# Kernel optimization log

Hardware: AMD Instinct MI355X
Metric: run time of the kernel (lower is better)

The kernel has to match this reference:

```python
import jax, jax.numpy as jnp
import numpy as np
import math

E = 2048         # n_embd
H = 16           # num query head pairs (num_heads)
HKV = 8          # num_kv_heads
NREP = H // HKV  # 2
HD = E // H // 2 # head_dim = 64
DEPTH = 12
LAMBDA_INIT = 0.8 - 0.6 * math.exp(-0.3 * DEPTH)
EPS = 1e-6


def setup_inputs() -> dict:
    key = jax.random.key(0)
    ks = jax.random.split(key, 10)
    s = lambda fan_in: 1.0 / np.sqrt(fan_in)
    return {
        "x": jax.random.normal(ks[0], (2, 2048, E), jnp.float32),
        "Wq": jax.random.normal(ks[1], (E, E), jnp.float32) * s(E),
        "Wk": jax.random.normal(ks[2], (E, E // NREP), jnp.float32) * s(E),
        "Wv": jax.random.normal(ks[3], (E, E // NREP), jnp.float32) * s(E),
        "Wo": jax.random.normal(ks[4], (E, E), jnp.float32) * s(E),
        "lam_q1": jax.random.normal(ks[5], (HD,), jnp.float32) * 0.1,
        "lam_k1": jax.random.normal(ks[6], (HD,), jnp.float32) * 0.1,
        "lam_q2": jax.random.normal(ks[7], (HD,), jnp.float32) * 0.1,
        "lam_k2": jax.random.normal(ks[8], (HD,), jnp.float32) * 0.1,
        "g": jnp.ones((2 * HD,), jnp.float32),  # RMSNorm weight
    }


def _rotary(x, cos, sin):
    # x: [B, T, nh, HD]; cos/sin: [T, HD//2]
    d = x.shape[-1] // 2
    x1, x2 = x[..., :d], x[..., d:]
    c = cos[None, :, None, :]
    si = sin[None, :, None, :]
    return jnp.concatenate([x1 * c + x2 * si, -x1 * si + x2 * c], axis=-1)


def reference(x, Wq, Wk, Wv, Wo, lam_q1, lam_k1, lam_q2, lam_k2, g):
    B, T, _ = x.shape
    q = (x @ Wq).reshape(B, T, 2 * H, HD)
    k = (x @ Wk).reshape(B, T, 2 * HKV, HD)
    v = (x @ Wv).reshape(B, T, HKV, 2 * HD)

    inv_freq = 1.0 / (10000.0 ** (jnp.arange(0, HD, 2, dtype=jnp.float32) / HD))
    freqs = jnp.arange(T, dtype=jnp.float32)[:, None] * inv_freq[None, :]
    cos, sin = jnp.cos(freqs), jnp.sin(freqs)
    q = _rotary(q, cos, sin)
    k = _rotary(k, cos, sin)

    q = jnp.transpose(q, (0, 2, 1, 3)) * (HD ** -0.5)   # [B, 2H, T, HD]
    k = jnp.repeat(jnp.transpose(k, (0, 2, 1, 3)), NREP, axis=1)  # [B, 2H, T, HD]
    v = jnp.repeat(jnp.transpose(v, (0, 2, 1, 3)), NREP, axis=1)  # [B, H, T, 2HD]

    scores = jnp.einsum('bhtd,bhsd->bhts', q, k)
    scores = jnp.nan_to_num(scores)
    mask = jnp.triu(jnp.full((T, T), -jnp.inf, scores.dtype), 1)
    scores = scores + mask
    p = jax.nn.softmax(scores.astype(jnp.float32), axis=-1).astype(scores.dtype)

    lam1 = jnp.exp(jnp.sum(lam_q1 * lam_k1))
    lam2 = jnp.exp(jnp.sum(lam_q2 * lam_k2))
    lam = lam1 - lam2 + LAMBDA_INIT

    p = p.reshape(B, H, 2, T, T)
    diff = p[:, :, 0] - lam * p[:, :, 1]               # [B, H, T, T]
    attn = jnp.einsum('bhts,bhsd->bhtd', diff, v)      # [B, H, T, 2HD]

    # RMSNorm over last dim (2*HD)
    attn = attn * jax.lax.rsqrt(jnp.mean(attn * attn, axis=-1, keepdims=True) + EPS) * g
    attn = attn * (1.0 - LAMBDA_INIT)
    attn = jnp.transpose(attn, (0, 2, 1, 3)).reshape(B, T, E)
    return attn @ Wo
```

## Files before the change

kernel.cpp:

```cpp
#include <hip/hip_runtime.h>

#define T_SEQ 2048

typedef __bf16 bf16x8 __attribute__((ext_vector_type(8)));
typedef float f32x4 __attribute__((ext_vector_type(4)));
typedef unsigned short u16;

__device__ __forceinline__ u16 f2b(float f) {
  unsigned u = __float_as_uint(f);
  unsigned r = 0x7fffu + ((u >> 16) & 1u);
  return (u16)((u + r) >> 16);
}
__device__ __forceinline__ float b2f(u16 v) {
  return __uint_as_float(((unsigned)v) << 16);
}
__device__ __forceinline__ f32x4 mfma16(bf16x8 a, bf16x8 b, f32x4 c) {
  return __builtin_amdgcn_mfma_f32_16x16x32_bf16(a, b, c, 0, 0, 0);
}
__device__ __forceinline__ unsigned pkhi(float lo, float hi) {
  return __builtin_amdgcn_perm(__float_as_uint(hi), __float_as_uint(lo), 0x07060302u);
}
#if defined(__has_builtin)
#if __has_builtin(__builtin_amdgcn_exp2f)
#define HAVE_RAW_EXP2 1
#endif
#endif
__device__ __forceinline__ float exp2r(float x) {
#ifdef HAVE_RAW_EXP2
  return __builtin_amdgcn_exp2f(x);
#else
  float r;
  asm("v_exp_f32 %0, %1" : "=v"(r) : "v"(x));
  return r;
#endif
}
__device__ __forceinline__ void glds16(const void* g, void* s) {
  __builtin_amdgcn_global_load_lds(
      (const __attribute__((address_space(1))) void*)(uintptr_t)g,
      (__attribute__((address_space(3))) void*)(unsigned)(uintptr_t)s, 16, 0, 0);
}

__global__ void lam_kernel(const float* __restrict__ q1, const float* __restrict__ k1,
                           const float* __restrict__ q2, const float* __restrict__ k2,
                           float* __restrict__ outp) {
  int l = threadIdx.x;
  float a = q1[l] * k1[l];
  float c = q2[l] * k2[l];
  #pragma unroll
  for (int off = 32; off > 0; off >>= 1) {
    a += __shfl_down(a, off);
    c += __shfl_down(c, off);
  }
  if (l == 0) outp[0] = expf(a) - expf(c) + 0.7836057665316244f;
}

__global__ __launch_bounds__(256) void convert_kernel(const float* __restrict__ in,
                                                      u16* __restrict__ outp, int n) {
  int i = (blockIdx.x * 256 + threadIdx.x) * 4;
  if (i >= n) return;
  float4 v = *(const float4*)(in + i);
  ushort4 pk;
  pk.x = f2b(v.x); pk.y = f2b(v.y); pk.z = f2b(v.z); pk.w = f2b(v.w);
  *(ushort4*)(outp + i) = pk;
}

__global__ __launch_bounds__(256) void transposeW_kernel(const float* __restrict__ Wq,
                                                         const float* __restrict__ Wk,
                                                         const float* __restrict__ Wv,
                                                         const float* __restrict__ Wo,
                                                         u16* __restrict__ outp) {
  __shared__ float tile[32][33];
  const int ro0 = blockIdx.y * 32;
  const int r0 = blockIdx.x * 32;
  const float* src; int C, cbase;
  if (ro0 < 2048)      { src = Wq; C = 2048; cbase = 0; }
  else if (ro0 < 3072) { src = Wk; C = 1024; cbase = 2048; }
  else if (ro0 < 4096) { src = Wv; C = 1024; cbase = 3072; }
  else                 { src = Wo; C = 2048; cbase = 4096; }
  const int cs0 = ro0 - cbase;
  const int tx = threadIdx.x & 31, ty = threadIdx.x >> 5;
  #pragma unroll
  for (int k2 = 0; k2 < 4; k2++)
    tile[ty * 4 + k2][tx] = src[(size_t)(r0 + ty * 4 + k2) * C + cs0 + tx];
  __syncthreads();
  #pragma unroll
  for (int k2 = 0; k2 < 4; k2++)
    outp[(size_t)(ro0 + ty * 4 + k2) * 2048 + r0 + tx] = f2b(tile[tx][ty * 4 + k2]);
}

#define STAGE_HALF(TILE, ROLE, BUF)                                                     \
  do {                                                                                  \
    const u16* sp_ = ((ROLE) == 0 || (ROLE) == 3 ? Ag : Bg) +                           \
                     (size_t)((ROLE) >= 2 ? 128 : 0) * K + (size_t)(TILE) * 64;         \
    u16* dp_ = ((ROLE) == 0 || (ROLE) == 3 ? &As[BUF][0] : &Bs[BUF][0]) +               \
               (((ROLE) >= 2 ? 128 : 0) + w * 8) * 64;                                  \
    glds16(sp_, dp_);                                                                   \
    glds16(sp_ + (size_t)64 * K, dp_ + 4096);                                           \
  } while (0)

#define PHASE(I, J, BUF, NEWA, NEWB, BN, STILE, SROLE, SBUF, DOVM)                      \
  do {                                                                                  \
    if (NEWA) {                                                                         \
      _Pragma("unroll") for (int u_ = 0; u_ < 4; u_++) {                                \
        const int ar_ = ((I) * 4 + u_) * 32 + wm * 16 + l15;                            \
        _Pragma("unroll") for (int kk_ = 0; kk_ < 2; kk_++)                             \
            am[u_][kk_] = *(const bf16x8*)&As[BUF][ar_ * 64 +                           \
                              (((kk_ * 4 + quad) ^ (ar_ & 7)) << 3)];                   \
      }                                                                                 \
    }                                                                                   \
    if (NEWB) {                                                                         \
      _Pragma("unroll") for (int v_ = 0; v_ < 2; v_++) {                                \
        const int br_ = ((J) * 2 + v_) * 64 + wn * 16 + l15;                            \
        _Pragma("unroll") for (int kk_ = 0; kk_ < 2; kk_++)                             \
            BN[v_][kk_] = *(const bf16x8*)&Bs[BUF][br_ * 64 +                           \
                              (((kk_ * 4 + quad) ^ (br_ & 7)) << 3)];                   \
      }                                                                                 \
    }                                                                                   \
    STAGE_HALF(STILE, SROLE, SBUF);                                                     \
    __builtin_amdgcn_s_barrier();                                                       \
    asm volatile("s_waitcnt lgkmcnt(0)" ::: "memory");                                  \
    __builtin_amdgcn_sched_barrier(0);                                                  \
    __builtin_amdgcn_s_setprio(1);                                                      \
    _Pragma("unroll") for (int u_ = 0; u_ < 4; u_++)                                    \
        _Pragma("unroll") for (int v_ = 0; v_ < 2; v_++) {                              \
      acc[(I) * 4 + u_][(J) * 2 + v_] =                                                 \
          mfma16(am[u_][0], BN[v_][0], acc[(I) * 4 + u_][(J) * 2 + v_]);                \
      acc[(I) * 4 + u_][(J) * 2 + v_] =                                                 \
          mfma16(am[u_][1], BN[v_][1], acc[(I) * 4 + u_][(J) * 2 + v_]);                \
    }                                                                                   \
    __builtin_amdgcn_s_setprio(0);                                                      \
    if (DOVM) asm volatile("s_waitcnt vmcnt(6)" ::: "memory");                          \
    __builtin_amdgcn_s_barrier();                                                       \
  } while (0)

__global__ __launch_bounds__(512, 2) void gemm256_kernel(const u16* __restrict__ A,
                                                         const u16* __restrict__ BT,
                                                         u16* __restrict__ C, int N, int K) {
  __shared__ alignas(16) u16 As[2][256 * 64];
  __shared__ alignas(16) u16 Bs[2][256 * 64];
  const int tid = threadIdx.x, w = tid >> 6, lane = tid & 63;
  const int l15 = lane & 15, quad = lane >> 4;
  const int wm = w >> 2, wn = w & 3;
  const int lr = lane >> 3, slot = lane & 7, csw = slot ^ lr;
  const int m0 = blockIdx.y * 256, n0 = blockIdx.x * 256;
  const int nkt = K >> 6;

  f32x4 acc[8][4];
  #pragma unroll
  for (int r = 0; r < 8; r++)
    #pragma unroll
    for (int s = 0; s < 4; s++) acc[r][s] = (f32x4){0.f, 0.f, 0.f, 0.f};

  const u16* Ag = A + (size_t)(m0 + w * 8 + lr) * K + csw * 8;
  const u16* Bg = BT + (size_t)(n0 + w * 8 + lr) * K + csw * 8;

  bf16x8 am[4][2], bn0[2][2], bn1[2][2];

  STAGE_HALF(0, 0, 0); STAGE_HALF(0, 1, 0); STAGE_HALF(0, 2, 0); STAGE_HALF(0, 3, 0);
  STAGE_HALF(1, 0, 1); STAGE_HALF(1, 1, 1); STAGE_HALF(1, 2, 1);
  asm volatile("s_waitcnt vmcnt(6)" ::: "memory");
  __builtin_amdgcn_s_barrier();

  #pragma unroll 1
  for (int t = 0; t < nkt; t += 2) {
    PHASE(0, 0, 0, 1, 1, bn0, t + 1, 3, 1, 0);
    PHASE(0, 1, 0, 0, 1, bn1, t + 2, 0, 0, 0);
    PHASE(1, 0, 0, 1, 0, bn0, t + 2, 1, 0, 0);
    PHASE(1, 1, 0, 0, 0, bn1, t + 2, 2, 0, 1);
    PHASE(0, 0, 1, 1, 1, bn0, t + 2, 3, 0, 0);
    PHASE(0, 1, 1, 0, 1, bn1, t + 3, 0, 1, 0);
    PHASE(1, 0, 1, 1, 0, bn0, t + 3, 1, 1, 0);
    PHASE(1, 1, 1, 0, 0, bn1, t + 3, 2, 1, 1);
  }

  const int crow = m0 + wm * 16 + quad * 4;
  const int ccol = n0 + wn * 16 + l15;
  #pragma unroll
  for (int r = 0; r < 8; r++)
    #pragma unroll
    for (int s = 0; s < 4; s++)
      #pragma unroll
      for (int rr = 0; rr < 4; rr++)
        C[(size_t)(crow + r * 32 + rr) * N + ccol + s * 64] = f2b(acc[r][s][rr]);
}

#define OSTAGE(TILE, CH, BUF)                                                           \
  do {                                                                                  \
    if ((CH) == 0) {                                                                    \
      glds16(Ag + (size_t)(TILE) * 64, &As[BUF][0] + w * 512);                          \
      glds16(Ag + (size_t)64 * K + (size_t)(TILE) * 64, &As[BUF][4096] + w * 512);      \
      glds16(Bg + (size_t)(TILE) * 64, &Bs[BUF][0] + w * 512);                          \
    } else {                                                                            \
      glds16(Bg + (size_t)64 * K + (size_t)(TILE) * 64, &Bs[BUF][4096] + w * 512);      \
      glds16(Bg + (size_t)128 * K + (size_t)(TILE) * 64, &Bs[BUF][8192] + w * 512);     \
      glds16(Bg + (size_t)192 * K + (size_t)(TILE) * 64, &Bs[BUF][12288] + w * 512);    \
    }                                                                                   \
  } while (0)

#define OPHASE(BUF, J, NEWA, STILE, SCH, SBUF, DOVM)                                    \
  do {                                                                                  \
    if (NEWA) {                                                                         \
      _Pragma("unroll") for (int fr_ = 0; fr_ < 4; fr_++) {                             \
        const int ar_ = wm * 64 + fr_ * 16 + l15;                                       \
        _Pragma("unroll") for (int kk_ = 0; kk_ < 2; kk_++)                             \
            am[fr_][kk_] = *(const bf16x8*)&As[BUF][ar_ * 64 +                          \
                               (((kk_ * 4 + quad) ^ (ar_ & 7)) << 3)];                  \
      }                                                                                 \
    }                                                                                   \
    _Pragma("unroll") for (int v_ = 0; v_ < 2; v_++) {                                  \
      const int br_ = ((J) * 2 + v_) * 64 + wn * 16 + l15;                              \
      _Pragma("unroll") for (int kk_ = 0; kk_ < 2; kk_++)                               \
          bn[v_][kk_] = *(const bf16x8*)&Bs[BUF][br_ * 64 +                             \
                            (((kk_ * 4 + quad) ^ (br_ & 7)) << 3)];                     \
    }                                                                                   \
    OSTAGE(STILE, SCH, SBUF);                                                           \
    __builtin_amdgcn_s_barrier();                                                       \
    asm volatile("s_waitcnt lgkmcnt(0)" ::: "memory");                                  \
    __builtin_amdgcn_sched_barrier(0);                                                  \
    __builtin_amdgcn_s_setprio(1);                                                      \
    _Pragma("unroll") for (int fr_ = 0; fr_ < 4; fr_++)                                 \
        _Pragma("unroll") for (int v_ = 0; v_ < 2; v_++) {                              \
      acc[fr_][(J) * 2 + v_] = mfma16(am[fr_][0], bn[v_][0], acc[fr_][(J) * 2 + v_]);   \
      acc[fr_][(J) * 2 + v_] = mfma16(am[fr_][1], bn[v_][1], acc[fr_][(J) * 2 + v_]);   \
    }                                                                                   \
    __builtin_amdgcn_s_setprio(0);                                                      \
    if (DOVM) asm volatile("s_waitcnt vmcnt(3)" ::: "memory");                          \
    __builtin_amdgcn_s_barrier();                                                       \
  } while (0)

__global__ __launch_bounds__(512, 2) void gemm128x256_kernel(const u16* __restrict__ A,
                                                             const u16* __restrict__ BT,
                                                             float* __restrict__ C,
                                                             int N, int K) {
  __shared__ alignas(16) u16 As[2][128 * 64];
  __shared__ alignas(16) u16 Bs[2][256 * 64];
  const int tid = threadIdx.x, w = tid >> 6, lane = tid & 63;
  const int l15 = lane & 15, quad = lane >> 4;
  const int wm = w >> 2, wn = w & 3;
  const int lr = lane >> 3, slot = lane & 7, csw = slot ^ lr;
  const int m0 = blockIdx.y * 128, n0 = blockIdx.x * 256;
  const int nkt = K >> 6;

  f32x4 acc[4][4];
  #pragma unroll
  for (int r = 0; r < 4; r++)
    #pragma unroll
    for (int s = 0; s < 4; s++) acc[r][s] = (f32x4){0.f, 0.f, 0.f, 0.f};

  const u16* Ag = A + (size_t)(m0 + w * 8 + lr) * K + csw * 8;
  const u16* Bg = BT + (size_t)(n0 + w * 8 + lr) * K + csw * 8;

  bf16x8 am[4][2], bn[2][2];

  OSTAGE(0, 0, 0); OSTAGE(0, 1, 0); OSTAGE(1, 0, 1);
  asm volatile("s_waitcnt vmcnt(3)" ::: "memory");
  __builtin_amdgcn_s_barrier();

  #pragma unroll 1
  for (int t = 0; t < nkt; t += 2) {
    OPHASE(0, 0, 1, t + 1, 1, 1, 0);
    OPHASE(0, 1, 0, t + 2, 0, 0, 1);
    OPHASE(1, 0, 1, t + 2, 1, 0, 0);
    OPHASE(1, 1, 0, t + 3, 0, 1, 1);
  }

  const int crow = m0 + wm * 64 + quad * 4;
  #pragma unroll
  for (int r = 0; r < 4; r++)
    #pragma unroll
    for (int s = 0; s < 4; s++) {
      const int col = n0 + s * 64 + wn * 16 + l15;
      #pragma unroll
      for (int rr = 0; rr < 4; rr++)
        C[(size_t)(crow + r * 16 + rr) * N + col] = acc[r][s][rr];
    }
}

__global__ __launch_bounds__(256) void rotab_kernel(float* __restrict__ ct,
                                                    float* __restrict__ st) {
  int idx = blockIdx.x * 256 + threadIdx.x;
  int i = idx & 31, t = idx >> 5;
  float invf = exp2f(-(float)i * 0.4152410118609203f);
  float ang = (float)t * invf;
  ct[idx] = cosf(ang);
  st[idx] = sinf(ang);
}

__global__ __launch_bounds__(256) void rotary_kernel(const u16* __restrict__ qkv,
                                                     const float* __restrict__ ct,
                                                     const float* __restrict__ st,
                                                     u16* __restrict__ Qb,
                                                     u16* __restrict__ Kb, float qscale) {
  int idx = blockIdx.x * 256 + threadIdx.x;
  int i4 = (idx & 7) * 4;
  int bt = (idx >> 3) & 4095;
  int hh = idx >> 15;
  int t = bt & (T_SEQ - 1), b = bt >> 11;
  bool isq = hh < 32;
  int col = isq ? hh * 64 : 2048 + (hh - 32) * 64;
  size_t inb = (size_t)bt * 4096 + col + i4;
  ushort4 xa = *(const ushort4*)(qkv + inb);
  ushort4 xb = *(const ushort4*)(qkv + inb + 32);
  float4 c4 = *(const float4*)(ct + t * 32 + i4);
  float4 s4 = *(const float4*)(st + t * 32 + i4);
  float scale = isq ? qscale : 1.0f;
  ushort4 o1, o2;
  {
    float x1 = b2f(xa.x), x2 = b2f(xb.x);
    o1.x = f2b((x1 * c4.x + x2 * s4.x) * scale);
    o2.x = f2b((x2 * c4.x - x1 * s4.x) * scale);
  }
  {
    float x1 = b2f(xa.y), x2 = b2f(xb.y);
    o1.y = f2b((x1 * c4.y + x2 * s4.y) * scale);
    o2.y = f2b((x2 * c4.y - x1 * s4.y) * scale);
  }
  {
    float x1 = b2f(xa.z), x2 = b2f(xb.z);
    o1.z = f2b((x1 * c4.z + x2 * s4.z) * scale);
    o2.z = f2b((x2 * c4.z - x1 * s4.z) * scale);
  }
  {
    float x1 = b2f(xa.w), x2 = b2f(xb.w);
    o1.w = f2b((x1 * c4.w + x2 * s4.w) * scale);
    o2.w = f2b((x2 * c4.w - x1 * s4.w) * scale);
  }
  u16* outp = isq ? (Qb + (size_t)(b * 32 + hh) * (T_SEQ * 64))
                  : (Kb + (size_t)(b * 16 + hh - 32) * (T_SEQ * 64));
  size_t ob = (size_t)t * 64 + i4;
  *(ushort4*)(outp + ob) = o1;
  *(ushort4*)(outp + ob + 32) = o2;
}

__global__ __launch_bounds__(256) void vtrans_kernel(const u16* __restrict__ qkv,
                                                     u16* __restrict__ outp) {
  __shared__ unsigned tile[32][33];
  int bh = blockIdx.z;
  int t0 = blockIdx.x * 32, dv0 = blockIdx.y * 32;
  int tx = threadIdx.x & 31, ty = threadIdx.x >> 5;
  int bt_base = (bh >> 3) * T_SEQ;
  int col = 3072 + (bh & 7) * 128 + dv0 + tx;
  #pragma unroll
  for (int k2 = 0; k2 < 4; k2++)
    tile[ty * 4 + k2][tx] = qkv[(size_t)(bt_base + t0 + ty * 4 + k2) * 4096 + col];
  __syncthreads();
  const int stile = t0 >> 6;
  const int sold = (t0 & 63) + tx;
  const int slo = sold & 31, hb = sold >> 5;
  const int sp = hb * 32 + ((slo >> 2) & 3) * 8 + ((slo >> 4) & 1) * 4 + (slo & 3);
  #pragma unroll
  for (int k2 = 0; k2 < 4; k2++) {
    int dv = dv0 + ty * 4 + k2;
    outp[(((size_t)bh * 32 + stile) * 128 + dv) * 64 + sp] = (u16)tile[tx][ty * 4 + k2];
  }
}

__global__ __launch_bounds__(256) void attn_kernel(const u16* __restrict__ Qb,
                                                   const u16* __restrict__ Kb,
                                                   const u16* __restrict__ Vt,
                                                   const float* __restrict__ lamp,
                                                   const float* __restrict__ g,
                                                   u16* __restrict__ attn_out) {
  __shared__ alignas(16) char smem[49152];
  u16* const Ks0 = (u16*)smem;
  u16* const Vs0 = (u16*)(smem + 16384);
  u16* const Psb = (u16*)smem;
  const int pr = blockIdx.x;
  const int bh = blockIdx.y;
  const int b = bh >> 4, h = bh & 15;
  const int tid = threadIdx.x, w = tid >> 6, lane = tid & 63;
  const int l15 = lane & 15, quad = lane >> 4;
  const int lr = lane >> 3, slot = lane & 7, csw = slot ^ lr;
  const float lam = lamp[0];

  union { unsigned u[4]; bf16x8 v; } onesu;
  onesu.u[0] = 0x3F803F80u; onesu.u[1] = 0x3F803F80u;
  onesu.u[2] = 0x3F803F80u; onesu.u[3] = 0x3F803F80u;
  const bf16x8 vone = onesu.v;

  const u16* Kg = Kb + (size_t)(b * 16 + h) * (T_SEQ * 64) + (w * 16 + lr) * 64 + csw * 8;
  const u16* Vg = Vt + (size_t)(b * 8 + (h >> 1)) * (T_SEQ * 128) + w * 2048 + lr * 64 + csw * 8;
  u16* kd[2] = {Ks0 + w * 1024, Ks0 + 4096 + w * 1024};
  u16* vd[2] = {Vs0 + w * 2048, Vs0 + 8192 + w * 2048};

  #pragma unroll 1
  for (int half = 0; half < 2; half++) {
    const int tt = half ? 31 - pr : pr;
    const int qb = tt * 64 + w * 16;
    const int qglob = qb + l15;

    bf16x8 qf[2][2];
    #pragma unroll
    for (int e = 0; e < 2; e++)
      #pragma unroll
      for (int kk = 0; kk < 2; kk++)
        qf[e][kk] = *(const bf16x8*)&Qb[((size_t)(b * 32 + 2 * h + e) * T_SEQ + qb + l15) * 64 +
                                        kk * 32 + quad * 8];

    f32x4 o[2][8];
    f32x4 lacc[2];
    #pragma unroll
    for (int e = 0; e < 2; e++) {
      lacc[e] = (f32x4){0.f, 0.f, 0.f, 0.f};
      #pragma unroll
      for (int nt = 0; nt < 8; nt++) o[e][nt] = (f32x4){0.f, 0.f, 0.f, 0.f};
    }

    {
      glds16(Kg, kd[0]); glds16(Kg + 512, kd[0] + 512);
      glds16(Vg, vd[0]); glds16(Vg + 512, vd[0] + 512);
      glds16(Vg + 1024, vd[0] + 1024); glds16(Vg + 1536, vd[0] + 1536);
    }
    __syncthreads();

    #pragma unroll 1
    for (int st = 0; st <= tt; st++) {
      const int buf = st & 1;
      const u16* Ksb = Ks0 + buf * 4096;
      const u16* Vsb = Vs0 + buf * 8192;
      if (st < tt) {
        const u16* kp = Kg + (size_t)(st + 1) * 4096;
        const u16* vp = Vg + (size_t)(st + 1) * 8192;
        glds16(kp, kd[buf ^ 1]); glds16(kp + 512, kd[buf ^ 1] + 512);
        glds16(vp, vd[buf ^ 1]); glds16(vp + 512, vd[buf ^ 1] + 512);
        glds16(vp + 1024, vd[buf ^ 1] + 1024); glds16(vp + 1536, vd[buf ^ 1] + 1536);
      }

      bf16x8 kf[4][2];
      #pragma unroll
      for (int j = 0; j < 4; j++) {
        const int rk = j * 16 + l15;
        #pragma unroll
        for (int kk = 0; kk < 2; kk++)
          kf[j][kk] = *(const bf16x8*)&Ksb[rk * 64 + (((kk * 4 + quad) ^ (rk & 7)) << 3)];
      }

      bf16x8 pa[2][2];
      #pragma unroll
      for (int e = 0; e < 2; e++) {
        f32x4 sc[4];
        __builtin_amdgcn_s_setprio(1);
        #pragma unroll
        for (int j = 0; j < 4; j++) {
          f32x4 z = {0.f, 0.f, 0.f, 0.f};
          z = mfma16(kf[j][0], qf[e][0], z);
          sc[j] = mfma16(kf[j][1], qf[e][1], z);
        }
        __builtin_amdgcn_s_setprio(0);
        if (st == tt) {
          #pragma unroll
          for (int j = 0; j < 4; j++) {
            int srow = st * 64 + j * 16 + quad * 4;
            #pragma unroll
            for (int rr = 0; rr < 4; rr++)
              if (srow + rr > qglob) sc[j][rr] = -1e30f;
          }
        }
        union { unsigned u[8]; bf16x8 v[2]; } pk;
        #pragma unroll
        for (int j = 0; j < 4; j++) {
          #pragma unroll
          for (int rr = 0; rr < 4; rr++) sc[j][rr] = exp2r(sc[j][rr]);
          pk.u[j * 2] = pkhi(sc[j][0], sc[j][1]);
          pk.u[j * 2 + 1] = pkhi(sc[j][2], sc[j][3]);
        }
        pa[e][0] = pk.v[0];
        pa[e][1] = pk.v[1];
        lacc[e] = mfma16(vone, pa[e][0], lacc[e]);
        lacc[e] = mfma16(vone, pa[e][1], lacc[e]);
      }
      __builtin_amdgcn_s_setprio(1);
      #pragma unroll
      for (int nt = 0; nt < 8; nt++) {
        const int rv = nt * 16 + l15;
        bf16x8 vf0 = *(const bf16x8*)&Vsb[rv * 64 + ((quad ^ (rv & 7)) << 3)];
        bf16x8 vf1 = *(const bf16x8*)&Vsb[rv * 64 + (((4 + quad) ^ (rv & 7)) << 3)];
        o[0][nt] = mfma16(vf0, pa[0][0], o[0][nt]);
        o[0][nt] = mfma16(vf1, pa[0][1], o[0][nt]);
        o[1][nt] = mfma16(vf0, pa[1][0], o[1][nt]);
        o[1][nt] = mfma16(vf1, pa[1][1], o[1][nt]);
      }
      __builtin_amdgcn_s_setprio(0);
      __syncthreads();
    }

    const float il0 = 1.f / lacc[0][0], il1 = lam / lacc[1][0];
    float ssq = 0.f;
    #pragma unroll
    for (int nt = 0; nt < 8; nt++)
      #pragma unroll
      for (int rr = 0; rr < 4; rr++) {
        float v = o[0][nt][rr] * il0 - o[1][nt][rr] * il1;
        o[0][nt][rr] = v;
        ssq += v * v;
      }
    ssq += __shfl_xor(ssq, 16);
    ssq += __shfl_xor(ssq, 32);
    const float rsc = rsqrtf(ssq * (1.f / 128.f) + 1e-6f) * 0.2163942334683756f;
    #pragma unroll
    for (int nt = 0; nt < 8; nt++) {
      float4 gv = *(const float4*)&g[nt * 16 + quad * 4];
      uint2 pk;
      pk.x = (unsigned)f2b(o[0][nt][0] * rsc * gv.x) |
             ((unsigned)f2b(o[0][nt][1] * rsc * gv.y) << 16);
      pk.y = (unsigned)f2b(o[0][nt][2] * rsc * gv.z) |
             ((unsigned)f2b(o[0][nt][3] * rsc * gv.w) << 16);
      *(uint2*)&Psb[(w * 16 + l15) * 136 + nt * 16 + quad * 4] = pk;
    }
    asm volatile("s_waitcnt lgkmcnt(0)" ::: "memory");
    __builtin_amdgcn_sched_barrier(0);
    #pragma unroll
    for (int i = 0; i < 4; i++) {
      const int r = (lane >> 4) + i * 4, c = (lane & 15) * 8;
      bf16x8 ov = *(const bf16x8*)&Psb[(w * 16 + r) * 136 + c];
      *(bf16x8*)&attn_out[(size_t)(b * T_SEQ + qb + r) * 2048 + h * 128 + c] = ov;
    }
    __syncthreads();
  }
}

extern "C" void kernel_launch(void* const* d_in, const int* in_sizes, int n_in, void* d_out,
                              int out_size, void* d_ws, size_t ws_size, hipStream_t stream) {
  const float* x = (const float*)d_in[0];
  const float* Wq = (const float*)d_in[1];
  const float* Wk = (const float*)d_in[2];
  const float* Wv = (const float*)d_in[3];
  const float* Wo = (const float*)d_in[4];
  const float* lq1 = (const float*)d_in[5];
  const float* lk1 = (const float*)d_in[6];
  const float* lq2 = (const float*)d_in[7];
  const float* lk2 = (const float*)d_in[8];
  const float* g = (const float*)d_in[9];

  char* ws = (char*)d_ws;
  u16* WT = (u16*)(ws);
  u16* xbf = (u16*)(ws + 25165824);
  u16* QKV = (u16*)(ws + 41943040);
  u16* Qb = (u16*)(ws + 75497472);
  u16* Kb = (u16*)(ws + 92274688);
  u16* Vt = (u16*)(ws + 100663296);
  u16* Attn = (u16*)(ws + 109051904);
  float* lam = (float*)(ws + 125829120);
  float* ct = (float*)(ws + 25165824);
  float* st = (float*)(ws + 25165824 + 262144);

  lam_kernel<<<1, 64, 0, stream>>>(lq1, lk1, lq2, lk2, lam);
  convert_kernel<<<8192, 256, 0, stream>>>(x, xbf, 8388608);
  transposeW_kernel<<<dim3(64, 192), 256, 0, stream>>>(Wq, Wk, Wv, Wo, WT);
  gemm256_kernel<<<dim3(16, 16), 512, 0, stream>>>(xbf, WT, QKV, 4096, 2048);
  rotab_kernel<<<256, 256, 0, stream>>>(ct, st);
  rotary_kernel<<<6144, 256, 0, stream>>>(QKV, ct, st, Qb, Kb, 0.18033688011112042f);
  vtrans_kernel<<<dim3(64, 4, 16), 256, 0, stream>>>(QKV, Vt);
  attn_kernel<<<dim3(16, 32), 256, 0, stream>>>(Qb, Kb, Vt, lam, g, Attn);
  gemm128x256_kernel<<<dim3(8, 32), 512, 0, stream>>>(Attn, WT + (size_t)4096 * 2048,
                                                      (float*)d_out, 2048, 2048);
}
```

Measured before the change: 313.6 us.

## Stage GEMM epilogues through LDS for coalesced stores; replace MFMA row-sum with VALU sum

The two GEMM kernels now write their accumulators into shared memory (reusing the operand buffers) and then issue wide, coalesced 16-byte row stores, replacing the scattered per-element global stores. Prefetch tile indices are clamped so out-of-range tiles are never read. In the attention kernel the softmax denominator is now accumulated with scalar adds plus cross-lane shuffles instead of extra MFMAs against a ones vector. The costs are extra LDS round trips and barriers in the epilogue, and the denominator now sums unrounded fp32 probabilities rather than the bf16 values fed to P·V.

```diff
diff --git a/kernel.cpp b/kernel.cpp
--- a/kernel.cpp
+++ b/kernel.cpp
@@ -90,8 +90,9 @@
 
 #define STAGE_HALF(TILE, ROLE, BUF)                                                     \
   do {                                                                                  \
+    const int tc_ = (TILE) < nkt ? (TILE) : (nkt - 1);                                  \
     const u16* sp_ = ((ROLE) == 0 || (ROLE) == 3 ? Ag : Bg) +                           \
-                     (size_t)((ROLE) >= 2 ? 128 : 0) * K + (size_t)(TILE) * 64;         \
+                     (size_t)((ROLE) >= 2 ? 128 : 0) * K + (size_t)tc_ * 64;            \
     u16* dp_ = ((ROLE) == 0 || (ROLE) == 3 ? &As[BUF][0] : &Bs[BUF][0]) +               \
                (((ROLE) >= 2 ? 128 : 0) + w * 8) * 64;                                  \
     glds16(sp_, dp_);                                                                   \
@@ -136,8 +137,9 @@
 __global__ __launch_bounds__(512, 2) void gemm256_kernel(const u16* __restrict__ A,
                                                          const u16* __restrict__ BT,
                                                          u16* __restrict__ C, int N, int K) {
-  __shared__ alignas(16) u16 As[2][256 * 64];
-  __shared__ alignas(16) u16 Bs[2][256 * 64];
+  __shared__ alignas(16) char smemG[131072];
+  u16 (*As)[256 * 64] = (u16(*)[256 * 64])smemG;
+  u16 (*Bs)[256 * 64] = (u16(*)[256 * 64])(smemG + 65536);
   const int tid = threadIdx.x, w = tid >> 6, lane = tid & 63;
   const int l15 = lane & 15, quad = lane >> 4;
   const int wm = w >> 2, wn = w & 3;
@@ -173,27 +175,46 @@
     PHASE(1, 1, 1, 0, 0, bn1, t + 3, 2, 1, 1);
   }
 
-  const int crow = m0 + wm * 16 + quad * 4;
-  const int ccol = n0 + wn * 16 + l15;
-  #pragma unroll
-  for (int r = 0; r < 8; r++)
-    #pragma unroll
-    for (int s = 0; s < 4; s++)
-      #pragma unroll
-      for (int rr = 0; rr < 4; rr++)
-        C[(size_t)(crow + r * 32 + rr) * N + ccol + s * 64] = f2b(acc[r][s][rr]);
+  asm volatile("s_waitcnt vmcnt(0)" ::: "memory");
+  __builtin_amdgcn_s_barrier();
+  u16* CsE = (u16*)smemG;
+  #pragma unroll
+  for (int ch = 0; ch < 2; ch++) {
+    #pragma unroll
+    for (int rj = 0; rj < 4; rj++) {
+      const int r = ch * 4 + rj;
+      const int lrow = wm * 16 + quad * 4 + rj * 32;
+      #pragma unroll
+      for (int s = 0; s < 4; s++) {
+        const int lcol = wn * 16 + l15 + s * 64;
+        #pragma unroll
+        for (int rr = 0; rr < 4; rr++)
+          CsE[(lrow + rr) * 264 + lcol] = f2b(acc[r][s][rr]);
+      }
+    }
+    __syncthreads();
+    #pragma unroll
+    for (int pass = 0; pass < 8; pass++) {
+      const int row = (tid >> 5) + pass * 16;
+      const int col8 = (tid & 31) * 8;
+      bf16x8 v = *(const bf16x8*)&CsE[row * 264 + col8];
+      *(bf16x8*)&C[(size_t)(m0 + ch * 128 + row) * N + n0 + col8] = v;
+    }
+    if (ch == 0) __syncthreads();
+  }
 }
 
 #define OSTAGE(TILE, CH, BUF)                                                           \
   do {                                                                                  \
+    const int tc_ = (TILE) < nkt ? (TILE) : (nkt - 1);                                  \
     if ((CH) == 0) {                                                                    \
-      glds16(Ag + (size_t)(TILE) * 64, &As[BUF][0] + w * 512);                          \
-      glds16(Ag + (size_t)64 * K + (size_t)(TILE) * 64, &As[BUF][4096] + w * 512);      \
-      glds16(Bg + (size_t)(TILE) * 64, &Bs[BUF][0] + w * 512);                          \
+      glds16(Ag + (size_t)tc_ * 64, &As[BUF][0] + w * 512);                             \
+      glds16(Ag + (size_t)64 * K + (size_t)tc_ * 64, &As[BUF][4096] + w * 512);         \
+      glds16(Bg + (size_t)tc_ * 64, &Bs[BUF][0] + w * 512);                             \
     } else {                                                                            \
-      glds16(Bg + (size_t)64 * K + (size_t)(TILE) * 64, &Bs[BUF][4096] + w * 512);      \
-      glds16(Bg + (size_t)128 * K + (size_t)(TILE) * 64, &Bs[BUF][8192] + w * 512);     \
-      glds16(Bg + (size_t)192 * K + (size_t)(TILE) * 64, &Bs[BUF][12288] + w * 512);    \
+      glds16(Bg + (size_t)64 * K + (size_t)tc_ * 64, &Bs[BUF][4096] + w * 512);         \
+      glds16(Bg + (size_t)128 * K + (size_t)tc_ * 64, &Bs[BUF][8192] + w * 512);        \
+      glds16(Bg + (size_t)192 * K + (size_t)tc_ * 64, &Bs[BUF][12288] + w * 512);       \
     }                                                                                   \
   } while (0)
 
@@ -232,8 +253,9 @@
                                                              const u16* __restrict__ BT,
                                                              float* __restrict__ C,
                                                              int N, int K) {
-  __shared__ alignas(16) u16 As[2][128 * 64];
-  __shared__ alignas(16) u16 Bs[2][256 * 64];
+  __shared__ alignas(16) char smemO[98304];
+  u16 (*As)[128 * 64] = (u16(*)[128 * 64])smemO;
+  u16 (*Bs)[256 * 64] = (u16(*)[256 * 64])(smemO + 32768);
   const int tid = threadIdx.x, w = tid >> 6, lane = tid & 63;
   const int l15 = lane & 15, quad = lane >> 4;
   const int wm = w >> 2, wn = w & 3;
@@ -264,16 +286,34 @@
     OPHASE(1, 1, 0, t + 3, 0, 1, 1);
   }
 
-  const int crow = m0 + wm * 64 + quad * 4;
-  #pragma unroll
-  for (int r = 0; r < 4; r++)
-    #pragma unroll
-    for (int s = 0; s < 4; s++) {
-      const int col = n0 + s * 64 + wn * 16 + l15;
-      #pragma unroll
-      for (int rr = 0; rr < 4; rr++)
-        C[(size_t)(crow + r * 16 + rr) * N + col] = acc[r][s][rr];
-    }
+  asm volatile("s_waitcnt vmcnt(0)" ::: "memory");
+  __builtin_amdgcn_s_barrier();
+  float* CsF = (float*)smemO;
+  #pragma unroll
+  for (int ch = 0; ch < 2; ch++) {
+    if (wm == ch) {
+      #pragma unroll
+      for (int r = 0; r < 4; r++) {
+        const int lrow = r * 16 + quad * 4;
+        #pragma unroll
+        for (int s = 0; s < 4; s++) {
+          const int lcol = wn * 16 + l15 + s * 64;
+          #pragma unroll
+          for (int rr = 0; rr < 4; rr++)
+            CsF[(lrow + rr) * 260 + lcol] = acc[r][s][rr];
+        }
+      }
+    }
+    __syncthreads();
+    #pragma unroll
+    for (int pass = 0; pass < 8; pass++) {
+      const int row = (tid >> 6) + pass * 8;
+      const int col4 = (tid & 63) * 4;
+      f32x4 v = *(const f32x4*)&CsF[row * 260 + col4];
+      *(f32x4*)&C[(size_t)(m0 + ch * 64 + row) * N + n0 + col4] = v;
+    }
+    if (ch == 0) __syncthreads();
+  }
 }
 
 __global__ __launch_bounds__(256) void rotab_kernel(float* __restrict__ ct,
@@ -373,11 +413,6 @@
   const int lr = lane >> 3, slot = lane & 7, csw = slot ^ lr;
   const float lam = lamp[0];
 
-  union { unsigned u[4]; bf16x8 v; } onesu;
-  onesu.u[0] = 0x3F803F80u; onesu.u[1] = 0x3F803F80u;
-  onesu.u[2] = 0x3F803F80u; onesu.u[3] = 0x3F803F80u;
-  const bf16x8 vone = onesu.v;
-
   const u16* Kg = Kb + (size_t)(b * 16 + h) * (T_SEQ * 64) + (w * 16 + lr) * 64 + csw * 8;
   const u16* Vg = Vt + (size_t)(b * 8 + (h >> 1)) * (T_SEQ * 128) + w * 2048 + lr * 64 + csw * 8;
   u16* kd[2] = {Ks0 + w * 1024, Ks0 + 4096 + w * 1024};
@@ -398,13 +433,11 @@
                                         kk * 32 + quad * 8];
 
     f32x4 o[2][8];
-    f32x4 lacc[2];
-    #pragma unroll
-    for (int e = 0; e < 2; e++) {
-      lacc[e] = (f32x4){0.f, 0.f, 0.f, 0.f};
+    float lsum[2] = {0.f, 0.f};
+    #pragma unroll
+    for (int e = 0; e < 2; e++)
       #pragma unroll
       for (int nt = 0; nt < 8; nt++) o[e][nt] = (f32x4){0.f, 0.f, 0.f, 0.f};
-    }
 
     {
       glds16(Kg, kd[0]); glds16(Kg + 512, kd[0] + 512);
@@ -456,18 +489,22 @@
               if (srow + rr > qglob) sc[j][rr] = -1e30f;
           }
         }
+        float ls = 0.f;
         union { unsigned u[8]; bf16x8 v[2]; } pk;
         #pragma unroll
         for (int j = 0; j < 4; j++) {
           #pragma unroll
-          for (int rr = 0; rr < 4; rr++) sc[j][rr] = exp2r(sc[j][rr]);
+          for (int rr = 0; rr < 4; rr++) {
+            float p = exp2r(sc[j][rr]);
+            sc[j][rr] = p;
+            ls += p;
+          }
           pk.u[j * 2] = pkhi(sc[j][0], sc[j][1]);
           pk.u[j * 2 + 1] = pkhi(sc[j][2], sc[j][3]);
         }
         pa[e][0] = pk.v[0];
         pa[e][1] = pk.v[1];
-        lacc[e] = mfma16(vone, pa[e][0], lacc[e]);
-        lacc[e] = mfma16(vone, pa[e][1], lacc[e]);
+        lsum[e] += ls;
       }
       __builtin_amdgcn_s_setprio(1);
       #pragma unroll
@@ -484,7 +521,10 @@
       __syncthreads();
     }
 
-    const float il0 = 1.f / lacc[0][0], il1 = lam / lacc[1][0];
+    float l0 = lsum[0], l1 = lsum[1];
+    l0 += __shfl_xor(l0, 16); l0 += __shfl_xor(l0, 32);
+    l1 += __shfl_xor(l1, 16); l1 += __shfl_xor(l1, 32);
+    const float il0 = 1.f / l0, il1 = lam / l1;
     float ssq = 0.f;
     #pragma unroll
     for (int nt = 0; nt < 8; nt++)
```

New measurement: 321.7 us. 1.03x slower.
